# Performance work log

Hardware: AMD Instinct MI355X
Metric: run time of the kernel (lower is better)

Reference implementation:

```python
import jax, jax.numpy as jnp
import numpy as np

GROUPSIZE = 128
ZERO_POINT = 8  # (maxq + 1) // 2 with maxq = 2**4 - 1


def setup_inputs() -> dict:
    key = jax.random.key(0)
    kA, ks, kq = jax.random.split(key, 3)
    M, K, N = 4096, 4096, 4096
    A = jax.random.normal(kA, (M, K), dtype=jnp.float32)
    # per-group scales, positive and small like real quantization scales
    s = jax.random.uniform(ks, (K // GROUPSIZE, N), dtype=jnp.float32) * 0.02 + 1e-3
    # int4 weights in [0, 15], packed 8 nibbles per int32 word along n
    nib = jax.random.randint(kq, (K, N), 0, 16, dtype=jnp.int32).astype(jnp.uint32)
    shifts = (4 * jnp.arange(8, dtype=jnp.uint32))
    q_u = (nib.reshape(K, N // 8, 8) << shifts).sum(axis=-1)  # uint32 (K, N//8)
    q = jax.lax.bitcast_convert_type(q_u, jnp.int32)
    return {"A": A, "s": s, "q": q}


def reference(A, s, q):
    # Unpack 8 int4 nibbles per int32 word: (K, N//8) -> (K, N)
    shifts = 4 * jnp.arange(8, dtype=jnp.int32)
    nib = (q[:, :, None] >> shifts) & 0xF  # (K, N//8, 8)
    nib = nib.reshape(q.shape[0], -1)      # (K, N)
    # Symmetric dequant with zero-point 8 and per-group (groupsize=128 rows) scales
    w = (nib.astype(A.dtype) - ZERO_POINT) * jnp.repeat(s.astype(A.dtype), GROUPSIZE, axis=0)
    return A @ w  # (M, N)
```

## Files before the change

kernel.cpp:

```cpp
#include <hip/hip_runtime.h>
#include <stdint.h>

#define GM 4096
#define GN 4096
#define GK 4096
#define QW (GN/8)

typedef __attribute__((ext_vector_type(4))) int   i32x4;
typedef __attribute__((ext_vector_type(8))) short bf16x8;
typedef __attribute__((ext_vector_type(4))) float f32x4;

#define AS1 __attribute__((address_space(1)))
#define AS3 __attribute__((address_space(3)))

static __device__ __forceinline__ void glds16(const void* g, void* l) {
  __builtin_amdgcn_global_load_lds((const AS1 uint32_t*)g, (AS3 uint32_t*)l, 16, 0, 0);
}

static __device__ __forceinline__ uint32_t bf16pack_rn(float hi, float lo) {
  uint32_t h = __float_as_uint(hi) + 0x8000u;
  uint32_t l = __float_as_uint(lo) + 0x8000u;
  return __builtin_amdgcn_perm(h, l, 0x07060302u);
}

static __device__ __forceinline__ uint32_t pack4i8(int b0, int b1, int b2, int b3) {
  return ((uint32_t)b0 & 255u) | (((uint32_t)b1 & 255u) << 8) |
         (((uint32_t)b2 & 255u) << 16) | (((uint32_t)b3 & 255u) << 24);
}

__global__ void __launch_bounds__(256) a_quant(const float* __restrict__ A,
                                               int8_t* __restrict__ Ai,
                                               float* __restrict__ ascale) {
  const int t    = threadIdx.x;
  const int lane = t & 63;
  const int row  = blockIdx.x * 4 + (t >> 6);
  const float* src = A + (size_t)row * GK;
  float4 v[16];
  float m = 0.f;
  #pragma unroll
  for (int i = 0; i < 16; ++i) {
    v[i] = *(const float4*)(src + i * 256 + lane * 4);
    m = fmaxf(m, fmaxf(fmaxf(fabsf(v[i].x), fabsf(v[i].y)),
                       fmaxf(fabsf(v[i].z), fabsf(v[i].w))));
  }
  #pragma unroll
  for (int off = 32; off >= 1; off >>= 1)
    m = fmaxf(m, __shfl_xor(m, off, 64));
  const float rmax = fmaxf(m, 1e-20f);
  const float inv  = 127.0f / rmax;
  #pragma unroll
  for (int i = 0; i < 16; ++i) {
    uint32_t b = pack4i8((int)__builtin_rintf(v[i].x * inv),
                         (int)__builtin_rintf(v[i].y * inv),
                         (int)__builtin_rintf(v[i].z * inv),
                         (int)__builtin_rintf(v[i].w * inv));
    *(uint32_t*)(Ai + (size_t)row * GK + i * 256 + lane * 4) = b;
  }
  if (lane == 0) ascale[row] = rmax * (1.0f / 127.0f);
}

__global__ void __launch_bounds__(256) w_scale(const float* __restrict__ S,
                                               float* __restrict__ wscale,
                                               float* __restrict__ winv) {
  const int n = blockIdx.x * 256 + threadIdx.x;
  float m = 0.f;
  #pragma unroll 8
  for (int g = 0; g < 32; ++g) m = fmaxf(m, S[(size_t)g * GN + n]);
  wscale[n] = m * (8.0f / 127.0f);
  winv[n]   = 127.0f / (8.0f * m);
}

__global__ void __launch_bounds__(256) w_quant(const float* __restrict__ S,
                                               const uint32_t* __restrict__ Q,
                                               const float* __restrict__ winv,
                                               int8_t* __restrict__ Wt) {
  __shared__ uint32_t T32[128 * 32];
  const int tid = threadIdx.x;
  const int n0  = blockIdx.x * 128;
  const int k0  = blockIdx.y * 128;
  const int g   = blockIdx.y;
  const int w   = tid & 15;
  const int kb  = tid >> 4;

  float r[8], c[8];
  {
    const float* sp = S + (size_t)g * GN + n0 + w * 8;
    const float* ip = winv + n0 + w * 8;
    float4 sa = *(const float4*)sp, sb = *(const float4*)(sp + 4);
    float4 ia = *(const float4*)ip, ib = *(const float4*)(ip + 4);
    const float sv[8] = {sa.x, sa.y, sa.z, sa.w, sb.x, sb.y, sb.z, sb.w};
    const float iv[8] = {ia.x, ia.y, ia.z, ia.w, ib.x, ib.y, ib.z, ib.w};
    #pragma unroll
    for (int j = 0; j < 8; ++j) { r[j] = sv[j] * iv[j]; c[j] = -8.0f * r[j]; }
  }

  const int swz = 4 * (w & 7);
  #pragma unroll
  for (int c2 = 0; c2 < 2; ++c2) {
    uint32_t q[4];
    #pragma unroll
    for (int i = 0; i < 4; ++i)
      q[i] = Q[(size_t)(k0 + c2 * 64 + kb * 4 + i) * QW + (n0 >> 3) + w];
    const int kword = c2 * 16 + kb;
    #pragma unroll
    for (int j = 0; j < 8; ++j) {
      int b[4];
      #pragma unroll
      for (int i = 0; i < 4; ++i) {
        float nib = (float)((q[i] >> (4 * j)) & 0xFu);
        b[i] = (int)__builtin_rintf(fmaf(nib, r[j], c[j]));
      }
      T32[(w * 8 + j) * 32 + (kword ^ swz)] = pack4i8(b[0], b[1], b[2], b[3]);
    }
  }
  __syncthreads();
  #pragma unroll
  for (int p = 0; p < 4; ++p) {
    int idx = p * 256 + tid;
    int n = idx >> 3, gr = idx & 7;
    uint4 v = *(const uint4*)(&T32[n * 32 + (gr ^ ((n >> 3) & 7)) * 4]);
    *(uint4*)(Wt + (size_t)(n0 + n) * GK + k0 + gr * 16) = v;
  }
}

__global__ void __launch_bounds__(512, 2) gemm_i8(const int8_t* __restrict__ Ai,
                                                  const int8_t* __restrict__ Wi,
                                                  const float* __restrict__ ascale,
                                                  const float* __restrict__ wscale,
                                                  float* __restrict__ C) {
  __shared__ __align__(16) int8_t As[2][256 * 128];
  __shared__ __align__(16) int8_t Bs[2][256 * 128];

  const int tid = threadIdx.x;
  const int bid = blockIdx.y * gridDim.x + blockIdx.x;
  const int swb = ((bid & 7) << 5) | (bid >> 3);
  const int m0  = (swb >> 4) * 256;
  const int n0  = (swb & 15) * 256;

  const int lane = tid & 63;
  const int wid  = tid >> 6;
  const int wm   = wid >> 2;
  const int wn   = wid & 3;
  const int col  = lane & 15;
  const int quad = lane >> 4;
  const int sw   = col & 7;

  const int ur0   = tid >> 3;
  const int pc    = tid & 7;
  const int qo    = ((pc ^ (ur0 & 7)) << 4);
  const int arow0 = ur0;
  const int brow0 = (ur0 & 31) + ((ur0 & 32) << 1);
  const size_t aoff = (size_t)(m0 + arow0) * GK + qo;
  const size_t boff = (size_t)(n0 + brow0) * GK + qo;
  const int dA0 = arow0 * 128 + pc * 16;
  const int dB0 = brow0 * 128 + pc * 16;

#define STAGE_A(b, kt, hi) do {                                              \
    const int8_t* s_ = Ai + aoff + (size_t)(hi) * 64 * GK + (size_t)(kt) * 128; \
    glds16(s_,                   &As[b][dA0 + (hi) * 8192]);                 \
    glds16(s_ + (size_t)128 * GK, &As[b][dA0 + (hi) * 8192 + 16384]);        \
  } while (0)
#define STAGE_B(b, kt, hi) do {                                              \
    const int8_t* s_ = Wi + boff + (size_t)(hi) * 32 * GK + (size_t)(kt) * 128; \
    glds16(s_,                   &Bs[b][dB0 + (hi) * 4096]);                 \
    glds16(s_ + (size_t)128 * GK, &Bs[b][dB0 + (hi) * 4096 + 16384]);        \
  } while (0)

  const int cq0 = ((quad    ) ^ sw) << 4;
  const int cq1 = ((quad + 4) ^ sw) << 4;
  const int aRd = (wm * 128 + col) * 128;
  const int bRd = (wn * 64  + col) * 128;

  i32x4 af[4][2], bf0[2][2], bf1[2][2];
  i32x4 acc[8][4];
  #pragma unroll
  for (int i = 0; i < 8; ++i)
    #pragma unroll
    for (int j = 0; j < 4; ++j)
      acc[i][j] = (i32x4){0, 0, 0, 0};

#define LDA_(b, h) do {                                                      \
    _Pragma("unroll")                                                        \
    for (int m_ = 0; m_ < 4; ++m_) {                                         \
      af[m_][0] = *(const i32x4*)(&As[b][aRd + (h) * 8192 + m_ * 2048 + cq0]); \
      af[m_][1] = *(const i32x4*)(&As[b][aRd + (h) * 8192 + m_ * 2048 + cq1]); \
    }                                                                        \
  } while (0)
#define LDB_(b, g, BF) do {                                                  \
    _Pragma("unroll")                                                        \
    for (int n_ = 0; n_ < 2; ++n_) {                                         \
      BF[n_][0] = *(const i32x4*)(&Bs[b][bRd + (g) * 4096 + n_ * 2048 + cq0]); \
      BF[n_][1] = *(const i32x4*)(&Bs[b][bRd + (g) * 4096 + n_ * 2048 + cq1]); \
    }                                                                        \
  } while (0)
#define MFMAQ_(h, g, BF) do {                                                \
    _Pragma("unroll")                                                        \
    for (int m_ = 0; m_ < 4; ++m_)                                           \
      _Pragma("unroll")                                                      \
      for (int n_ = 0; n_ < 2; ++n_) {                                       \
        acc[(h)*4+m_][(g)*2+n_] = __builtin_amdgcn_mfma_i32_16x16x64_i8(     \
            af[m_][0], BF[n_][0], acc[(h)*4+m_][(g)*2+n_], 0, 0, 0);         \
        acc[(h)*4+m_][(g)*2+n_] = __builtin_amdgcn_mfma_i32_16x16x64_i8(     \
            af[m_][1], BF[n_][1], acc[(h)*4+m_][(g)*2+n_], 0, 0, 0);         \
      }                                                                      \
  } while (0)
#define BAR()   __builtin_amdgcn_s_barrier()
#define LGKM0() asm volatile("s_waitcnt lgkmcnt(0)" ::: "memory")
#define VM6()   asm volatile("s_waitcnt vmcnt(6)" ::: "memory")

  STAGE_A(0, 0, 0); STAGE_A(0, 0, 1); STAGE_B(0, 0, 0); STAGE_B(0, 0, 1);
  STAGE_A(1, 1, 0); STAGE_B(1, 1, 0); STAGE_B(1, 1, 1);
  VM6();
  BAR();

  for (int it = 0; it < GK / 256; ++it) {
    const int t1 = 2 * it + 1;
    const int t2 = (2 * it + 2) & 31;
    const int t3 = (2 * it + 3) & 31;

    LDA_(0, 0); LDB_(0, 0, bf0);
    STAGE_A(1, t1, 1);
    BAR(); LGKM0();
    __builtin_amdgcn_s_setprio(1); MFMAQ_(0, 0, bf0); __builtin_amdgcn_s_setprio(0);
    BAR();
    LDB_(0, 1, bf1);
    STAGE_A(0, t2, 0);
    BAR(); LGKM0();
    __builtin_amdgcn_s_setprio(1); MFMAQ_(0, 1, bf1); __builtin_amdgcn_s_setprio(0);
    BAR();
    LDA_(0, 1);
    STAGE_B(0, t2, 0);
    BAR(); LGKM0();
    __builtin_amdgcn_s_setprio(1); MFMAQ_(1, 1, bf1); __builtin_amdgcn_s_setprio(0);
    BAR();
    STAGE_B(0, t2, 1);
    BAR(); LGKM0();
    __builtin_amdgcn_s_setprio(1); MFMAQ_(1, 0, bf0); __builtin_amdgcn_s_setprio(0);
    VM6();
    BAR();
    LDA_(1, 0); LDB_(1, 0, bf0);
    STAGE_A(0, t2, 1);
    BAR(); LGKM0();
    __builtin_amdgcn_s_setprio(1); MFMAQ_(0, 0, bf0); __builtin_amdgcn_s_setprio(0);
    BAR();
    LDB_(1, 1, bf1);
    STAGE_A(1, t3, 0);
    BAR(); LGKM0();
    __builtin_amdgcn_s_setprio(1); MFMAQ_(0, 1, bf1); __builtin_amdgcn_s_setprio(0);
    BAR();
    LDA_(1, 1);
    STAGE_B(1, t3, 0);
    BAR(); LGKM0();
    __builtin_amdgcn_s_setprio(1); MFMAQ_(1, 1, bf1); __builtin_amdgcn_s_setprio(0);
    BAR();
    STAGE_B(1, t3, 1);
    BAR(); LGKM0();
    __builtin_amdgcn_s_setprio(1); MFMAQ_(1, 0, bf0); __builtin_amdgcn_s_setprio(0);
    VM6();
    BAR();
  }

  #pragma unroll
  for (int h = 0; h < 2; ++h)
    #pragma unroll
    for (int m = 0; m < 4; ++m) {
      const int rbase = m0 + wm * 128 + h * 64 + m * 16 + quad * 4;
      float4 a4 = *(const float4*)(ascale + rbase);
      const float ar[4] = {a4.x, a4.y, a4.z, a4.w};
      #pragma unroll
      for (int g = 0; g < 2; ++g)
        #pragma unroll
        for (int n = 0; n < 2; ++n) {
          const int cbase = n0 + wn * 64 + g * 32 + n * 16 + col;
          const float ws = wscale[cbase];
          #pragma unroll
          for (int r = 0; r < 4; ++r)
            C[(size_t)(rbase + r) * GN + cbase]
              = (float)acc[h * 4 + m][g * 2 + n][r] * (ar[r] * ws);
        }
    }
#undef STAGE_A
#undef STAGE_B
#undef LDA_
#undef LDB_
#undef MFMAQ_
#undef BAR
#undef LGKM0
#undef VM6
}

#define BM 128
#define BN 128
#define BK 32

__global__ void __launch_bounds__(256) w4a32_gemm(
    const float* __restrict__ A,
    const float* __restrict__ S,
    const uint32_t* __restrict__ Q,
    float* __restrict__ C)
{
  __shared__ __align__(16) ushort As[BM*BK];
  __shared__ __align__(16) ushort Bs[BN*BK];

  const int tid  = threadIdx.x;
  const int m0   = blockIdx.y*BM;
  const int n0   = blockIdx.x*BN;
  const int wcol  = tid & 15;
  const int kpair = tid >> 4;
  const int ln   = tid & 63;
  const int wid  = tid >> 6;
  const int wm   = (wid >> 1) * 64;
  const int wn   = (wid & 1) * 64;
  const int col  = ln & 15;
  const int quad = ln >> 4;

  f32x4 acc[4][4];
  #pragma unroll
  for (int i=0;i<4;++i)
    #pragma unroll
    for (int j=0;j<4;++j)
      acc[i][j] = (f32x4){0.f,0.f,0.f,0.f};

  float sv[8], cv[8];
  float4 spf0, spf1;

  const float*    Abase = A + (size_t)m0 * GK;
  const uint32_t* Qbase = Q + (size_t)(n0>>3) + wcol;

  {
    const float* sp = S + n0 + wcol*8;
    spf0 = *(const float4*)sp;
    spf1 = *(const float4*)(sp + 4);
  }

  float4 a4[4];
  uint32_t wqa, wqb;
  #pragma unroll
  for (int i=0;i<4;++i) {
    int f = tid + i*256;
    a4[i] = *(const float4*)(Abase + (size_t)(f>>3)*GK + ((f&7)*4));
  }
  wqa = Qbase[(size_t)(2*kpair)   * QW];
  wqb = Qbase[(size_t)(2*kpair+1) * QW];

  for (int k0 = 0; k0 < GK; k0 += BK) {
    if ((k0 & 127) == 0) {
      sv[0]=spf0.x; sv[1]=spf0.y; sv[2]=spf0.z; sv[3]=spf0.w;
      sv[4]=spf1.x; sv[5]=spf1.y; sv[6]=spf1.z; sv[7]=spf1.w;
      #pragma unroll
      for (int j=0;j<8;++j) cv[j] = -8.0f * sv[j];
    }

    #pragma unroll
    for (int i=0;i<4;++i) {
      int f = tid + i*256;
      int row = f>>3, c4 = f&7;
      *(uint2*)(&As[row*BK + c4*4]) =
        make_uint2(bf16pack_rn(a4[i].y, a4[i].x), bf16pack_rn(a4[i].w, a4[i].z));
    }

    {
      const int kk = (2*kpair) ^ (8*(wcol&3));
      #pragma unroll
      for (int j=0;j<8;++j) {
        float fa = (float)((wqa >> (4*j)) & 0xFu);
        float fb = (float)((wqb >> (4*j)) & 0xFu);
        float wa = fmaf(fa, sv[j], cv[j]);
        float wb = fmaf(fb, sv[j], cv[j]);
        int n = wcol*8 + j;
        *(uint32_t*)(&Bs[n*BK + kk]) = bf16pack_rn(wb, wa);
      }
    }

    int kn = k0 + BK; if (kn >= GK) kn = 0;
    if ((kn & 127) == 0) {
      const float* sp = S + (size_t)(kn>>7)*GN + n0 + wcol*8;
      spf0 = *(const float4*)sp;
      spf1 = *(const float4*)(sp + 4);
    }
    #pragma unroll
    for (int i=0;i<4;++i) {
      int f = tid + i*256;
      a4[i] = *(const float4*)(Abase + (size_t)(f>>3)*GK + kn + ((f&7)*4));
    }
    wqa = Qbase[(size_t)(kn + 2*kpair)   * QW];
    wqb = Qbase[(size_t)(kn + 2*kpair+1) * QW];

    __syncthreads();

    bf16x8 af[4], bfr[4];
    #pragma unroll
    for (int t=0;t<4;++t) {
      af[t] = *(const bf16x8*)(&As[(wm + t*16 + col)*BK + quad*8]);
      int n = wn + t*16 + col;
      int kk = (quad*8) ^ (8*((n>>3)&3));
      bfr[t] = *(const bf16x8*)(&Bs[n*BK + kk]);
    }
    #pragma unroll
    for (int mt=0;mt<4;++mt)
      #pragma unroll
      for (int nt=0;nt<4;++nt)
        acc[mt][nt] = __builtin_amdgcn_mfma_f32_16x16x32_bf16(
                          af[mt], bfr[nt], acc[mt][nt], 0, 0, 0);

    __syncthreads();
  }

  #pragma unroll
  for (int mt=0;mt<4;++mt)
    #pragma unroll
    for (int nt=0;nt<4;++nt)
      #pragma unroll
      for (int r=0;r<4;++r)
        C[(size_t)(m0 + wm + mt*16 + quad*4 + r)*GN + n0 + wn + nt*16 + col]
          = acc[mt][nt][r];
}

extern "C" void kernel_launch(void* const* d_in, const int* in_sizes, int n_in,
                              void* d_out, int out_size, void* d_ws, size_t ws_size,
                              hipStream_t stream) {
  const float*    A = (const float*)d_in[0];
  const float*    S = (const float*)d_in[1];
  const uint32_t* Q = (const uint32_t*)d_in[2];
  float*          C = (float*)d_out;

  const size_t need = (size_t)GM * GK + (size_t)GN * GK + 3 * 4096 * 4 + 4096;
  if (ws_size >= need) {
    int8_t* Ai  = (int8_t*)d_ws;
    int8_t* Wt  = Ai + (size_t)GM * GK;
    float* ascale = (float*)(Wt + (size_t)GN * GK);
    float* wscale = ascale + 4096;
    float* winv   = wscale + 4096;
    a_quant<<<dim3(GM / 4), dim3(256), 0, stream>>>(A, Ai, ascale);
    w_scale<<<dim3(GN / 256), dim3(256), 0, stream>>>(S, wscale, winv);
    w_quant<<<dim3(GN / 128, GK / 128), dim3(256), 0, stream>>>(S, Q, winv, Wt);
    gemm_i8<<<dim3(GN / 256, GM / 256), dim3(512), 0, stream>>>(Ai, Wt, ascale, wscale, C);
  } else {
    w4a32_gemm<<<dim3(GN / BN, GM / BM), dim3(256), 0, stream>>>(A, S, Q, C);
  }
}
```

Measured before the change: 193.1 us.

## Fuse quantization prep kernels into one launch and trim GEMM loop barriers

Merges the activation quantization, weight-scale and weight-quantization kernels into a single `prep` kernel whose blocks branch on their index. Each weight-quant block now computes its own per-column scale maxima in shared memory instead of reading a precomputed `winv` buffer. This removes two launches and the serialization between them, at the cost of some redundant scale reductions. In the int8 GEMM main loop it drops the explicit lgkmcnt(0) waits and half the barriers, and issues the global->LDS staging ahead of the LDS fragment reads. Ordering is left to compiler-inserted waits, which gives more overlap but risks LDS hazards if the remaining barriers are not enough.

```diff
diff --git a/kernel.cpp b/kernel.cpp
--- a/kernel.cpp
+++ b/kernel.cpp
@@ -28,98 +28,127 @@
          (((uint32_t)b2 & 255u) << 16) | (((uint32_t)b3 & 255u) << 24);
 }
 
-__global__ void __launch_bounds__(256) a_quant(const float* __restrict__ A,
-                                               int8_t* __restrict__ Ai,
-                                               float* __restrict__ ascale) {
-  const int t    = threadIdx.x;
-  const int lane = t & 63;
-  const int row  = blockIdx.x * 4 + (t >> 6);
-  const float* src = A + (size_t)row * GK;
-  float4 v[16];
-  float m = 0.f;
-  #pragma unroll
-  for (int i = 0; i < 16; ++i) {
-    v[i] = *(const float4*)(src + i * 256 + lane * 4);
-    m = fmaxf(m, fmaxf(fmaxf(fabsf(v[i].x), fabsf(v[i].y)),
-                       fmaxf(fabsf(v[i].z), fabsf(v[i].w))));
-  }
-  #pragma unroll
-  for (int off = 32; off >= 1; off >>= 1)
-    m = fmaxf(m, __shfl_xor(m, off, 64));
-  const float rmax = fmaxf(m, 1e-20f);
-  const float inv  = 127.0f / rmax;
-  #pragma unroll
-  for (int i = 0; i < 16; ++i) {
-    uint32_t b = pack4i8((int)__builtin_rintf(v[i].x * inv),
-                         (int)__builtin_rintf(v[i].y * inv),
-                         (int)__builtin_rintf(v[i].z * inv),
-                         (int)__builtin_rintf(v[i].w * inv));
-    *(uint32_t*)(Ai + (size_t)row * GK + i * 256 + lane * 4) = b;
-  }
-  if (lane == 0) ascale[row] = rmax * (1.0f / 127.0f);
-}
-
-__global__ void __launch_bounds__(256) w_scale(const float* __restrict__ S,
-                                               float* __restrict__ wscale,
-                                               float* __restrict__ winv) {
-  const int n = blockIdx.x * 256 + threadIdx.x;
-  float m = 0.f;
-  #pragma unroll 8
-  for (int g = 0; g < 32; ++g) m = fmaxf(m, S[(size_t)g * GN + n]);
-  wscale[n] = m * (8.0f / 127.0f);
-  winv[n]   = 127.0f / (8.0f * m);
-}
-
-__global__ void __launch_bounds__(256) w_quant(const float* __restrict__ S,
-                                               const uint32_t* __restrict__ Q,
-                                               const float* __restrict__ winv,
-                                               int8_t* __restrict__ Wt) {
+__global__ void __launch_bounds__(256) prep(const float* __restrict__ A,
+                                            const float* __restrict__ S,
+                                            const uint32_t* __restrict__ Q,
+                                            int8_t* __restrict__ Ai,
+                                            float* __restrict__ ascale,
+                                            int8_t* __restrict__ Wt,
+                                            float* __restrict__ wscale) {
   __shared__ uint32_t T32[128 * 32];
+  __shared__ float4   red[8][32];
+  __shared__ float    winv_l[128];
+
+  const int b   = blockIdx.x;
   const int tid = threadIdx.x;
-  const int n0  = blockIdx.x * 128;
-  const int k0  = blockIdx.y * 128;
-  const int g   = blockIdx.y;
-  const int w   = tid & 15;
-  const int kb  = tid >> 4;
-
-  float r[8], c[8];
-  {
-    const float* sp = S + (size_t)g * GN + n0 + w * 8;
-    const float* ip = winv + n0 + w * 8;
-    float4 sa = *(const float4*)sp, sb = *(const float4*)(sp + 4);
-    float4 ia = *(const float4*)ip, ib = *(const float4*)(ip + 4);
-    const float sv[8] = {sa.x, sa.y, sa.z, sa.w, sb.x, sb.y, sb.z, sb.w};
-    const float iv[8] = {ia.x, ia.y, ia.z, ia.w, ib.x, ib.y, ib.z, ib.w};
-    #pragma unroll
-    for (int j = 0; j < 8; ++j) { r[j] = sv[j] * iv[j]; c[j] = -8.0f * r[j]; }
-  }
-
-  const int swz = 4 * (w & 7);
-  #pragma unroll
-  for (int c2 = 0; c2 < 2; ++c2) {
-    uint32_t q[4];
-    #pragma unroll
-    for (int i = 0; i < 4; ++i)
-      q[i] = Q[(size_t)(k0 + c2 * 64 + kb * 4 + i) * QW + (n0 >> 3) + w];
-    const int kword = c2 * 16 + kb;
-    #pragma unroll
-    for (int j = 0; j < 8; ++j) {
-      int b[4];
-      #pragma unroll
-      for (int i = 0; i < 4; ++i) {
-        float nib = (float)((q[i] >> (4 * j)) & 0xFu);
-        b[i] = (int)__builtin_rintf(fmaf(nib, r[j], c[j]));
+
+  if (b < 1024) {
+    const int lane = tid & 63;
+    const int row  = b * 4 + (tid >> 6);
+    const float* src = A + (size_t)row * GK;
+    float4 v[16];
+    float m = 0.f;
+    #pragma unroll
+    for (int i = 0; i < 16; ++i) {
+      v[i] = *(const float4*)(src + i * 256 + lane * 4);
+      m = fmaxf(m, fmaxf(fmaxf(fabsf(v[i].x), fabsf(v[i].y)),
+                         fmaxf(fabsf(v[i].z), fabsf(v[i].w))));
+    }
+    #pragma unroll
+    for (int off = 32; off >= 1; off >>= 1)
+      m = fmaxf(m, __shfl_xor(m, off, 64));
+    const float rmax = fmaxf(m, 1e-20f);
+    const float inv  = 127.0f / rmax;
+    #pragma unroll
+    for (int i = 0; i < 16; ++i) {
+      uint32_t bb = pack4i8((int)__builtin_rintf(v[i].x * inv),
+                            (int)__builtin_rintf(v[i].y * inv),
+                            (int)__builtin_rintf(v[i].z * inv),
+                            (int)__builtin_rintf(v[i].w * inv));
+      *(uint32_t*)(Ai + (size_t)row * GK + i * 256 + lane * 4) = bb;
+    }
+    if (lane == 0) ascale[row] = rmax * (1.0f / 127.0f);
+  } else if (b < 2048) {
+    const int wb = b - 1024;
+    const int n0 = (wb & 31) * 128;
+    const int k0 = (wb >> 5) * 128;
+    const int g  = wb >> 5;
+    const int w  = tid & 15;
+    const int kb = tid >> 4;
+
+    {
+      const int c4 = tid & 31;
+      const int g8 = tid >> 5;
+      float4 m4 = make_float4(0.f, 0.f, 0.f, 0.f);
+      #pragma unroll
+      for (int gg = 0; gg < 4; ++gg) {
+        float4 sv = *(const float4*)(S + (size_t)(g8 * 4 + gg) * GN + n0 + c4 * 4);
+        m4.x = fmaxf(m4.x, sv.x); m4.y = fmaxf(m4.y, sv.y);
+        m4.z = fmaxf(m4.z, sv.z); m4.w = fmaxf(m4.w, sv.w);
       }
-      T32[(w * 8 + j) * 32 + (kword ^ swz)] = pack4i8(b[0], b[1], b[2], b[3]);
-    }
-  }
-  __syncthreads();
-  #pragma unroll
-  for (int p = 0; p < 4; ++p) {
-    int idx = p * 256 + tid;
-    int n = idx >> 3, gr = idx & 7;
-    uint4 v = *(const uint4*)(&T32[n * 32 + (gr ^ ((n >> 3) & 7)) * 4]);
-    *(uint4*)(Wt + (size_t)(n0 + n) * GK + k0 + gr * 16) = v;
+      red[g8][c4] = m4;
+      __syncthreads();
+      if (g8 == 0) {
+        float4 m = red[0][c4];
+        #pragma unroll
+        for (int rr = 1; rr < 8; ++rr) {
+          float4 o = red[rr][c4];
+          m.x = fmaxf(m.x, o.x); m.y = fmaxf(m.y, o.y);
+          m.z = fmaxf(m.z, o.z); m.w = fmaxf(m.w, o.w);
+        }
+        winv_l[c4 * 4 + 0] = 127.0f / (8.0f * m.x);
+        winv_l[c4 * 4 + 1] = 127.0f / (8.0f * m.y);
+        winv_l[c4 * 4 + 2] = 127.0f / (8.0f * m.z);
+        winv_l[c4 * 4 + 3] = 127.0f / (8.0f * m.w);
+      }
+      __syncthreads();
+    }
+
+    float r[8], c[8];
+    {
+      const float* sp = S + (size_t)g * GN + n0 + w * 8;
+      float4 sa = *(const float4*)sp, sb = *(const float4*)(sp + 4);
+      float4 ia = *(const float4*)&winv_l[w * 8];
+      float4 ib = *(const float4*)&winv_l[w * 8 + 4];
+      const float sv[8] = {sa.x, sa.y, sa.z, sa.w, sb.x, sb.y, sb.z, sb.w};
+      const float iv[8] = {ia.x, ia.y, ia.z, ia.w, ib.x, ib.y, ib.z, ib.w};
+      #pragma unroll
+      for (int j = 0; j < 8; ++j) { r[j] = sv[j] * iv[j]; c[j] = -8.0f * r[j]; }
+    }
+
+    const int swz = 4 * (w & 7);
+    #pragma unroll
+    for (int c2 = 0; c2 < 2; ++c2) {
+      uint32_t q[4];
+      #pragma unroll
+      for (int i = 0; i < 4; ++i)
+        q[i] = Q[(size_t)(k0 + c2 * 64 + kb * 4 + i) * QW + (n0 >> 3) + w];
+      const int kword = c2 * 16 + kb;
+      #pragma unroll
+      for (int j = 0; j < 8; ++j) {
+        int bb[4];
+        #pragma unroll
+        for (int i = 0; i < 4; ++i) {
+          float nib = (float)((q[i] >> (4 * j)) & 0xFu);
+          bb[i] = (int)__builtin_rintf(fmaf(nib, r[j], c[j]));
+        }
+        T32[(w * 8 + j) * 32 + (kword ^ swz)] = pack4i8(bb[0], bb[1], bb[2], bb[3]);
+      }
+    }
+    __syncthreads();
+    #pragma unroll
+    for (int p = 0; p < 4; ++p) {
+      int idx = p * 256 + tid;
+      int n = idx >> 3, gr = idx & 7;
+      uint4 v = *(const uint4*)(&T32[n * 32 + (gr ^ ((n >> 3) & 7)) * 4]);
+      *(uint4*)(Wt + (size_t)(n0 + n) * GK + k0 + gr * 16) = v;
+    }
+  } else {
+    const int n = (b - 2048) * 256 + tid;
+    float m = 0.f;
+    #pragma unroll 8
+    for (int gg = 0; gg < 32; ++gg) m = fmaxf(m, S[(size_t)gg * GN + n]);
+    wscale[n] = m * (8.0f / 127.0f);
   }
 }
 
@@ -205,8 +234,9 @@
       }                                                                      \
   } while (0)
 #define BAR()   __builtin_amdgcn_s_barrier()
-#define LGKM0() asm volatile("s_waitcnt lgkmcnt(0)" ::: "memory")
 #define VM6()   asm volatile("s_waitcnt vmcnt(6)" ::: "memory")
+#define PRIO1() __builtin_amdgcn_s_setprio(1)
+#define PRIO0() __builtin_amdgcn_s_setprio(0)
 
   STAGE_A(0, 0, 0); STAGE_A(0, 0, 1); STAGE_B(0, 0, 0); STAGE_B(0, 0, 1);
   STAGE_A(1, 1, 0); STAGE_B(1, 1, 0); STAGE_B(1, 1, 1);
@@ -218,44 +248,36 @@
     const int t2 = (2 * it + 2) & 31;
     const int t3 = (2 * it + 3) & 31;
 
+    STAGE_A(1, t1, 1);
     LDA_(0, 0); LDB_(0, 0, bf0);
-    STAGE_A(1, t1, 1);
-    BAR(); LGKM0();
-    __builtin_amdgcn_s_setprio(1); MFMAQ_(0, 0, bf0); __builtin_amdgcn_s_setprio(0);
-    BAR();
+    PRIO1(); MFMAQ_(0, 0, bf0); PRIO0();
+    BAR();
+    STAGE_A(0, t2, 0);
     LDB_(0, 1, bf1);
-    STAGE_A(0, t2, 0);
-    BAR(); LGKM0();
-    __builtin_amdgcn_s_setprio(1); MFMAQ_(0, 1, bf1); __builtin_amdgcn_s_setprio(0);
-    BAR();
+    PRIO1(); MFMAQ_(0, 1, bf1); PRIO0();
+    BAR();
+    STAGE_B(0, t2, 0);
     LDA_(0, 1);
-    STAGE_B(0, t2, 0);
-    BAR(); LGKM0();
-    __builtin_amdgcn_s_setprio(1); MFMAQ_(1, 1, bf1); __builtin_amdgcn_s_setprio(0);
+    PRIO1(); MFMAQ_(1, 1, bf1); PRIO0();
     BAR();
     STAGE_B(0, t2, 1);
-    BAR(); LGKM0();
-    __builtin_amdgcn_s_setprio(1); MFMAQ_(1, 0, bf0); __builtin_amdgcn_s_setprio(0);
+    PRIO1(); MFMAQ_(1, 0, bf0); PRIO0();
     VM6();
     BAR();
+    STAGE_A(0, t2, 1);
     LDA_(1, 0); LDB_(1, 0, bf0);
-    STAGE_A(0, t2, 1);
-    BAR(); LGKM0();
-    __builtin_amdgcn_s_setprio(1); MFMAQ_(0, 0, bf0); __builtin_amdgcn_s_setprio(0);
-    BAR();
+    PRIO1(); MFMAQ_(0, 0, bf0); PRIO0();
+    BAR();
+    STAGE_A(1, t3, 0);
     LDB_(1, 1, bf1);
-    STAGE_A(1, t3, 0);
-    BAR(); LGKM0();
-    __builtin_amdgcn_s_setprio(1); MFMAQ_(0, 1, bf1); __builtin_amdgcn_s_setprio(0);
-    BAR();
+    PRIO1(); MFMAQ_(0, 1, bf1); PRIO0();
+    BAR();
+    STAGE_B(1, t3, 0);
     LDA_(1, 1);
-    STAGE_B(1, t3, 0);
-    BAR(); LGKM0();
-    __builtin_amdgcn_s_setprio(1); MFMAQ_(1, 1, bf1); __builtin_amdgcn_s_setprio(0);
+    PRIO1(); MFMAQ_(1, 1, bf1); PRIO0();
     BAR();
     STAGE_B(1, t3, 1);
-    BAR(); LGKM0();
-    __builtin_amdgcn_s_setprio(1); MFMAQ_(1, 0, bf0); __builtin_amdgcn_s_setprio(0);
+    PRIO1(); MFMAQ_(1, 0, bf0); PRIO0();
     VM6();
     BAR();
   }
@@ -285,8 +307,9 @@
 #undef LDB_
 #undef MFMAQ_
 #undef BAR
-#undef LGKM0
 #undef VM6
+#undef PRIO1
+#undef PRIO0
 }
 
 #define BM 128
@@ -430,10 +453,7 @@
     int8_t* Wt  = Ai + (size_t)GM * GK;
     float* ascale = (float*)(Wt + (size_t)GN * GK);
     float* wscale = ascale + 4096;
-    float* winv   = wscale + 4096;
-    a_quant<<<dim3(GM / 4), dim3(256), 0, stream>>>(A, Ai, ascale);
-    w_scale<<<dim3(GN / 256), dim3(256), 0, stream>>>(S, wscale, winv);
-    w_quant<<<dim3(GN / 128, GK / 128), dim3(256), 0, stream>>>(S, Q, winv, Wt);
+    prep<<<dim3(1024 + 1024 + 16), dim3(256), 0, stream>>>(A, S, Q, Ai, ascale, Wt, wscale);
     gemm_i8<<<dim3(GN / 256, GM / 256), dim3(512), 0, stream>>>(Ai, Wt, ascale, wscale, C);
   } else {
     w4a32_gemm<<<dim3(GN / BN, GM / BM), dim3(256), 0, stream>>>(A, S, Q, C);
```

Result: faster. 183.8 us (-4.8%).
